# Performance work log

Measured on AMD Instinct MI355X. Metric: run time of the kernel, lower is better.

## Reference

```python
import jax, jax.numpy as jnp
import numpy as np

N_NODES = 100000
N_EDGES = 1600000
D_IN = 64
D_HID = 64


def setup_inputs() -> dict:
    key = jax.random.key(0)
    k1, k2, k3, k4, k5 = jax.random.split(key, 5)
    x = jax.random.normal(k1, (N_NODES, D_IN), dtype=jnp.float32)
    edge_index = jax.random.randint(k2, (2, N_EDGES), 0, N_NODES, dtype=jnp.int64)
    edge_weight = jax.random.uniform(k3, (N_EDGES,), dtype=jnp.float32)
    # GCNConv glorot-initialized linear weights (bias=False)
    s0 = (6.0 / (D_IN + D_HID)) ** 0.5
    W0 = jax.random.uniform(k4, (D_IN, D_HID), minval=-s0, maxval=s0, dtype=jnp.float32)
    s1 = (6.0 / (D_HID + D_HID)) ** 0.5
    W1 = jax.random.uniform(k5, (D_HID, D_HID), minval=-s1, maxval=s1, dtype=jnp.float32)
    return {"x": x, "edge_index": edge_index, "edge_weight": edge_weight, "W0": W0, "W1": W1}


def _gcn_layer(x, W, src, dst, edge_weight, deg_inv_sqrt, n_nodes):
    # h = X W  (bias=False)
    h = x @ W  # [N, D]
    # symmetric normalization including self-loops (weight 1)
    norm = deg_inv_sqrt[src] * edge_weight * deg_inv_sqrt[dst]  # [E]
    # gather src features, scale, scatter-sum at dst
    agg = jax.ops.segment_sum(norm[:, None] * h[src], dst, num_segments=n_nodes)
    # self-loop contribution: norm_ii = deg_inv_sqrt[i]^2 * 1
    agg = agg + (deg_inv_sqrt * deg_inv_sqrt)[:, None] * h
    return jax.nn.relu(agg)  # dropout is identity in eval mode


def reference(x, edge_index, edge_weight, W0, W1):
    src, dst = edge_index[0], edge_index[1]
    # degree with self-loops (self-loop weight = 1), aggregated at dst (source_to_target flow)
    deg = jax.ops.segment_sum(edge_weight, dst, num_segments=N_NODES) + 1.0
    deg_inv_sqrt = jax.lax.rsqrt(deg)
    x = _gcn_layer(x, W0, src, dst, edge_weight, deg_inv_sqrt, N_NODES)
    x = _gcn_layer(x, W1, src, dst, edge_weight, deg_inv_sqrt, N_NODES)
    return x
```

## Files before the change

kernel.cpp:

```cpp
#include <hip/hip_runtime.h>
#include <hip/hip_fp16.h>

#define D 64
#define BSH 9
#define BSZ (1 << BSH)
#define PB 4096
#define CAPR 18432
#define CAPU (2 * CAPR)
#define SCAP 9216

__global__ __launch_bounds__(256) void initcur(int* __restrict__ ccur, int nbuck) {
    int t = threadIdx.x;
    if (t < nbuck) ccur[t] = t * CAPR;
}

__global__ __launch_bounds__(512) void bucket1(const int* __restrict__ src,
                                               const int* __restrict__ dst,
                                               const float* __restrict__ ew,
                                               int* __restrict__ ccur,
                                               int2* __restrict__ pairs2,
                                               int E, int nbuck) {
    __shared__ int hist[512];
    __shared__ int lbase[512];
    __shared__ int gbase[512];
    __shared__ int w0s[PB];
    __shared__ int w1s[PB];
    __shared__ unsigned char bids[PB];
    int t = threadIdx.x;
    hist[t] = 0;
    __syncthreads();
    int e0 = blockIdx.x * PB;
    int cnt = min(PB, E - e0);
    int b[8], lr[8], w0[8], w1[8];
    int i8 = t * 8;
    bool full8 = (i8 + 8 <= cnt);
    if (full8) {
        int4   sa = *(const int4*)&src[e0 + i8];
        int4   sb = *(const int4*)&src[e0 + i8 + 4];
        int4   da = *(const int4*)&dst[e0 + i8];
        int4   db = *(const int4*)&dst[e0 + i8 + 4];
        float4 wa = *(const float4*)&ew[e0 + i8];
        float4 wb = *(const float4*)&ew[e0 + i8 + 4];
        int ss[8] = {sa.x, sa.y, sa.z, sa.w, sb.x, sb.y, sb.z, sb.w};
        int ds[8] = {da.x, da.y, da.z, da.w, db.x, db.y, db.z, db.w};
        float wv[8] = {wa.x, wa.y, wa.z, wa.w, wb.x, wb.y, wb.z, wb.w};
#pragma unroll
        for (int k = 0; k < 8; ++k) {
            b[k]  = ds[k] >> BSH;
            w0[k] = ss[k] | ((ds[k] & (BSZ - 1)) << 17);
            w1[k] = __float_as_int(wv[k]);
            lr[k] = atomicAdd(&hist[b[k]], 1);
        }
    } else {
#pragma unroll
        for (int k = 0; k < 8; ++k) {
            int idx = i8 + k;
            if (idx < cnt) {
                int d = dst[e0 + idx];
                b[k]  = d >> BSH;
                w0[k] = src[e0 + idx] | ((d & (BSZ - 1)) << 17);
                w1[k] = __float_as_int(ew[e0 + idx]);
                lr[k] = atomicAdd(&hist[b[k]], 1);
            }
        }
    }
    __syncthreads();
    int hv = hist[t];
    lbase[t] = hv;
    __syncthreads();
    for (int off = 1; off < 512; off <<= 1) {
        int u = (t >= off) ? lbase[t - off] : 0;
        __syncthreads();
        lbase[t] += u;
        __syncthreads();
    }
    int excl = lbase[t] - hv;
    __syncthreads();
    lbase[t] = excl;
    if (t < nbuck && hv > 0) gbase[t] = atomicAdd(&ccur[t], hv);
    __syncthreads();
#pragma unroll
    for (int k = 0; k < 8; ++k) {
        int idx = i8 + k;
        if (idx < cnt) {
            int slot = lbase[b[k]] + lr[k];
            w0s[slot] = w0[k];
            w1s[slot] = w1[k];
            bids[slot] = (unsigned char)b[k];
        }
    }
    __syncthreads();
    for (int i = t; i < cnt; i += 512) {
        int bb = bids[i];
        int pos = gbase[bb] + (i - lbase[bb]);
        pairs2[pos] = make_int2(w0s[i], w1s[i]);
    }
}

__global__ __launch_bounds__(512) void sort2(int2* __restrict__ pairs2,
                                             unsigned int* __restrict__ pairsU,
                                             const int* __restrict__ ccur,
                                             int2* __restrict__ rng,
                                             float* __restrict__ dis,
                                             int N, int nbuck) {
    __shared__ int2 se[SCAP];
    __shared__ int cnt[512];
    __shared__ float sdeg[512];
    __shared__ int lb[512];
    __shared__ int cur[512];
    int b = blockIdx.x;
    int t = threadIdx.x;
    int baseR = b * CAPR;
    int baseU = b * CAPU;
    int cntb = min(ccur[b] - baseR, SCAP);
    for (int i = t; i < cntb; i += 512) se[i] = pairs2[baseR + i];
    cnt[t] = 0;
    sdeg[t] = 0.0f;
    __syncthreads();
    for (int i = t; i < cntb; i += 512) {
        int2 p = se[i];
        int dl = p.x >> 17;
        atomicAdd(&cnt[dl], 1);
        atomicAdd(&sdeg[dl], __int_as_float(p.y));
    }
    __syncthreads();
    int node = (b << BSH) + t;
    int pc = (node < N) ? ((cnt[t] + 1 + 31) & ~31) : 0;
    lb[t] = pc;
    __syncthreads();
    for (int off = 1; off < 512; off <<= 1) {
        int u = (t >= off) ? lb[t - off] : 0;
        __syncthreads();
        lb[t] += u;
        __syncthreads();
    }
    int excl = lb[t] - pc;
    int totalPad = lb[511];
    float dloc = rsqrtf(sdeg[t] + 1.0f);
    __syncthreads();
    sdeg[t] = dloc;
    cur[t]  = baseU + excl;
    if (node < N) {
        rng[node] = make_int2(baseU + excl, baseU + excl + pc);
        dis[node] = dloc;
    }
    for (int i = t; i < totalPad; i += 512) pairsU[baseU + i] = 0u;
    __syncthreads();
    for (int i = t; i < cntb; i += 512) {
        int2 p = se[i];
        int dl = p.x >> 17;
        int s  = p.x & 0x1FFFF;
        int pos = atomicAdd(&cur[dl], 1);
        float w = __int_as_float(p.y) * sdeg[dl];
        unsigned int h = (unsigned int)__half_as_ushort(__float2half_rn(w));
        pairsU[pos] = ((unsigned int)s << 15) | ((h + 1u) >> 1);
    }
    __syncthreads();
    if (node < N) {
        unsigned int h = (unsigned int)__half_as_ushort(__float2half_rn(dloc));
        pairsU[cur[t]] = ((unsigned int)node << 15) | ((h + 1u) >> 1);
    }
}

__global__ __launch_bounds__(256) void gemm64h(const float* __restrict__ X,
                                               const float* __restrict__ W,
                                               const float* __restrict__ dis,
                                               __half* __restrict__ Hb, int n) {
    __shared__ float Ws[64 * 64];
    __shared__ float Xs[16 * 64];
    for (int t = threadIdx.x; t < 64 * 64; t += 256) Ws[t] = W[t];
    int row0 = blockIdx.x * 16;
    for (int t = threadIdx.x; t < 16 * 64; t += 256) {
        int r = row0 + (t >> 6);
        Xs[t] = (r < n) ? X[r * 64 + (t & 63)] : 0.0f;
    }
    __syncthreads();
    int r  = threadIdx.x >> 4;
    int jc = (threadIdx.x & 15) * 4;
    float4 acc = make_float4(0.f, 0.f, 0.f, 0.f);
#pragma unroll
    for (int k = 0; k < 64; ++k) {
        float xv = Xs[r * 64 + k];
        float4 w = *(const float4*)&Ws[k * 64 + jc];
        acc.x += xv * w.x; acc.y += xv * w.y; acc.z += xv * w.z; acc.w += xv * w.w;
    }
    int rr = row0 + r;
    if (rr < n) {
        float ds = dis[rr];
        ushort4 pk;
        pk.x = __half_as_ushort(__float2half(ds * acc.x));
        pk.y = __half_as_ushort(__float2half(ds * acc.y));
        pk.z = __half_as_ushort(__float2half(ds * acc.z));
        pk.w = __half_as_ushort(__float2half(ds * acc.w));
        *(ushort4*)&Hb[rr * 64 + jc] = pk;
    }
}

__global__ __launch_bounds__(256) void gather64(const unsigned int* __restrict__ pairs,
                                                const int2* __restrict__ rng,
                                                const __half* __restrict__ Hb,
                                                float* __restrict__ OUT, int N) {
    int node = blockIdx.x * 4 + (threadIdx.x >> 6);
    if (node >= N) return;
    int lane = threadIdx.x & 63;
    int g    = lane >> 3;
    int fl   = (lane & 7) * 8;
    int2 be = rng[node];
    __half2 z = __float2half2_rn(0.0f);
    __half2 a0[4] = {z, z, z, z};
    __half2 a1[4] = {z, z, z, z};
    __half2 a2[4] = {z, z, z, z};
    __half2 a3[4] = {z, z, z, z};
    for (int e = be.x; e < be.y; e += 32) {
        unsigned int pv = pairs[e + (lane & 31)];
        unsigned int q0 = __shfl(pv, g, 64);
        unsigned int q1 = __shfl(pv, g + 8, 64);
        unsigned int q2 = __shfl(pv, g + 16, 64);
        unsigned int q3 = __shfl(pv, g + 24, 64);
        uint4 r0 = *(const uint4*)(Hb + (size_t)(q0 >> 15) * 64 + fl);
        uint4 r1 = *(const uint4*)(Hb + (size_t)(q1 >> 15) * 64 + fl);
        uint4 r2 = *(const uint4*)(Hb + (size_t)(q2 >> 15) * 64 + fl);
        uint4 r3 = *(const uint4*)(Hb + (size_t)(q3 >> 15) * 64 + fl);
        __half2 w0 = __half2half2(__ushort_as_half((unsigned short)((q0 & 0x7FFFu) << 1)));
        __half2 w1 = __half2half2(__ushort_as_half((unsigned short)((q1 & 0x7FFFu) << 1)));
        __half2 w2 = __half2half2(__ushort_as_half((unsigned short)((q2 & 0x7FFFu) << 1)));
        __half2 w3 = __half2half2(__ushort_as_half((unsigned short)((q3 & 0x7FFFu) << 1)));
        const __half2* h0 = (const __half2*)&r0;
        const __half2* h1 = (const __half2*)&r1;
        const __half2* h2 = (const __half2*)&r2;
        const __half2* h3 = (const __half2*)&r3;
#pragma unroll
        for (int k = 0; k < 4; ++k) {
            a0[k] = __hfma2(w0, h0[k], a0[k]);
            a1[k] = __hfma2(w1, h1[k], a1[k]);
            a2[k] = __hfma2(w2, h2[k], a2[k]);
            a3[k] = __hfma2(w3, h3[k], a3[k]);
        }
    }
    __half2 a[4];
#pragma unroll
    for (int k = 0; k < 4; ++k)
        a[k] = __hadd2(__hadd2(a0[k], a1[k]), __hadd2(a2[k], a3[k]));
#pragma unroll
    for (int m = 8; m < 64; m <<= 1) {
#pragma unroll
        for (int k = 0; k < 4; ++k) {
            unsigned u = __shfl_xor(*(unsigned*)&a[k], m, 64);
            a[k] = __hadd2(a[k], *(__half2*)&u);
        }
    }
    if (g < 2) {
        int o = g * 2;
        float2 f0 = __half22float2(a[o]);
        float2 f1 = __half22float2(a[o + 1]);
        float4 vv;
        vv.x = fmaxf(f0.x, 0.0f);
        vv.y = fmaxf(f0.y, 0.0f);
        vv.z = fmaxf(f1.x, 0.0f);
        vv.w = fmaxf(f1.y, 0.0f);
        *(float4*)&OUT[node * 64 + fl + g * 4] = vv;
    }
}

extern "C" void kernel_launch(void* const* d_in, const int* in_sizes, int n_in,
                              void* d_out, int out_size, void* d_ws, size_t ws_size,
                              hipStream_t stream) {
    const float* x  = (const float*)d_in[0];
    const int*   ei = (const int*)d_in[1];
    const float* ew = (const float*)d_in[2];
    const float* W0 = (const float*)d_in[3];
    const float* W1 = (const float*)d_in[4];
    float* out = (float*)d_out;

    const int N = in_sizes[0] / D;
    const int E = in_sizes[2];
    const int* src = ei;
    const int* dst = ei + E;

    const int nbuck = (N + BSZ - 1) >> BSH;
    const int Na = (N + 1 + 255) & ~255;

    float* dis     = (float*)d_ws;
    int2*  rng     = (int2*)((int*)d_ws + Na);
    int*   ccur    = (int*)d_ws + 3 * Na;
    int2*  pairs2  = (int2*)((int*)d_ws + 3 * Na + 1024);
    unsigned int* pairsU = (unsigned int*)pairs2;
    __half* Hb     = (__half*)((int*)d_ws + 3 * Na + 1024 + (size_t)nbuck * CAPU);

    const int nb1 = (E + PB - 1) / PB;

    initcur<<<1, 256, 0, stream>>>(ccur, nbuck);
    bucket1<<<nb1, 512, 0, stream>>>(src, dst, ew, ccur, pairs2, E, nbuck);
    sort2<<<nbuck, 512, 0, stream>>>(pairs2, pairsU, ccur, rng, dis, N, nbuck);

    const int gemm_grid   = (N + 15) / 16;
    const int gather_grid = (N + 3) / 4;

    gemm64h<<<gemm_grid, 256, 0, stream>>>(x, W0, dis, Hb, N);
    gather64<<<gather_grid, 256, 0, stream>>>(pairsU, rng, Hb, out, N);

    gemm64h<<<gemm_grid, 256, 0, stream>>>(out, W1, dis, Hb, N);
    gather64<<<gather_grid, 256, 0, stream>>>(pairsU, rng, Hb, out, N);
}
```

Measured before the change: 195.7 us.

## Make gather persistent and process two nodes per wave for overlapped loads

The gather kernel now launches a fixed grid of 8192 waves that loop over nodes with a grid-stride. Each iteration handles two nodes and issues the first edge chunk of both before finishing either, aiming to overlap the latency of the irregular gathers. The four separate per-slot accumulators become one chained accumulator per node, which serialises the FMA dependencies. The first chunk is read unconditionally, which relies on padded pair storage or on nodes always having edges.

```diff
diff --git a/kernel.cpp b/kernel.cpp
--- a/kernel.cpp
+++ b/kernel.cpp
@@ -8,6 +8,7 @@
 #define CAPR 18432
 #define CAPU (2 * CAPR)
 #define SCAP 9216
+#define GWAVES 8192
 
 __global__ __launch_bounds__(256) void initcur(int* __restrict__ ccur, int nbuck) {
     int t = threadIdx.x;
@@ -196,51 +197,36 @@
     }
 }
 
-__global__ __launch_bounds__(256) void gather64(const unsigned int* __restrict__ pairs,
-                                                const int2* __restrict__ rng,
-                                                const __half* __restrict__ Hb,
-                                                float* __restrict__ OUT, int N) {
-    int node = blockIdx.x * 4 + (threadIdx.x >> 6);
-    if (node >= N) return;
-    int lane = threadIdx.x & 63;
-    int g    = lane >> 3;
-    int fl   = (lane & 7) * 8;
-    int2 be = rng[node];
-    __half2 z = __float2half2_rn(0.0f);
-    __half2 a0[4] = {z, z, z, z};
-    __half2 a1[4] = {z, z, z, z};
-    __half2 a2[4] = {z, z, z, z};
-    __half2 a3[4] = {z, z, z, z};
-    for (int e = be.x; e < be.y; e += 32) {
-        unsigned int pv = pairs[e + (lane & 31)];
-        unsigned int q0 = __shfl(pv, g, 64);
-        unsigned int q1 = __shfl(pv, g + 8, 64);
-        unsigned int q2 = __shfl(pv, g + 16, 64);
-        unsigned int q3 = __shfl(pv, g + 24, 64);
-        uint4 r0 = *(const uint4*)(Hb + (size_t)(q0 >> 15) * 64 + fl);
-        uint4 r1 = *(const uint4*)(Hb + (size_t)(q1 >> 15) * 64 + fl);
-        uint4 r2 = *(const uint4*)(Hb + (size_t)(q2 >> 15) * 64 + fl);
-        uint4 r3 = *(const uint4*)(Hb + (size_t)(q3 >> 15) * 64 + fl);
-        __half2 w0 = __half2half2(__ushort_as_half((unsigned short)((q0 & 0x7FFFu) << 1)));
-        __half2 w1 = __half2half2(__ushort_as_half((unsigned short)((q1 & 0x7FFFu) << 1)));
-        __half2 w2 = __half2half2(__ushort_as_half((unsigned short)((q2 & 0x7FFFu) << 1)));
-        __half2 w3 = __half2half2(__ushort_as_half((unsigned short)((q3 & 0x7FFFu) << 1)));
-        const __half2* h0 = (const __half2*)&r0;
-        const __half2* h1 = (const __half2*)&r1;
-        const __half2* h2 = (const __half2*)&r2;
-        const __half2* h3 = (const __half2*)&r3;
-#pragma unroll
-        for (int k = 0; k < 4; ++k) {
-            a0[k] = __hfma2(w0, h0[k], a0[k]);
-            a1[k] = __hfma2(w1, h1[k], a1[k]);
-            a2[k] = __hfma2(w2, h2[k], a2[k]);
-            a3[k] = __hfma2(w3, h3[k], a3[k]);
-        }
-    }
-    __half2 a[4];
-#pragma unroll
-    for (int k = 0; k < 4; ++k)
-        a[k] = __hadd2(__hadd2(a0[k], a1[k]), __hadd2(a2[k], a3[k]));
+__device__ __forceinline__ void acc_group(unsigned int pv, int g, int fl,
+                                          const __half* __restrict__ Hb,
+                                          __half2 a[4]) {
+    unsigned int q0 = __shfl(pv, g, 64);
+    unsigned int q1 = __shfl(pv, g + 8, 64);
+    unsigned int q2 = __shfl(pv, g + 16, 64);
+    unsigned int q3 = __shfl(pv, g + 24, 64);
+    uint4 r0 = *(const uint4*)(Hb + (size_t)(q0 >> 15) * 64 + fl);
+    uint4 r1 = *(const uint4*)(Hb + (size_t)(q1 >> 15) * 64 + fl);
+    uint4 r2 = *(const uint4*)(Hb + (size_t)(q2 >> 15) * 64 + fl);
+    uint4 r3 = *(const uint4*)(Hb + (size_t)(q3 >> 15) * 64 + fl);
+    __half2 w0 = __half2half2(__ushort_as_half((unsigned short)((q0 & 0x7FFFu) << 1)));
+    __half2 w1 = __half2half2(__ushort_as_half((unsigned short)((q1 & 0x7FFFu) << 1)));
+    __half2 w2 = __half2half2(__ushort_as_half((unsigned short)((q2 & 0x7FFFu) << 1)));
+    __half2 w3 = __half2half2(__ushort_as_half((unsigned short)((q3 & 0x7FFFu) << 1)));
+    const __half2* h0 = (const __half2*)&r0;
+    const __half2* h1 = (const __half2*)&r1;
+    const __half2* h2 = (const __half2*)&r2;
+    const __half2* h3 = (const __half2*)&r3;
+#pragma unroll
+    for (int k = 0; k < 4; ++k) {
+        a[k] = __hfma2(w0, h0[k], a[k]);
+        a[k] = __hfma2(w1, h1[k], a[k]);
+        a[k] = __hfma2(w2, h2[k], a[k]);
+        a[k] = __hfma2(w3, h3[k], a[k]);
+    }
+}
+
+__device__ __forceinline__ void finish_node(__half2 a[4], int g, int fl,
+                                            float* __restrict__ OUT, int node) {
 #pragma unroll
     for (int m = 8; m < 64; m <<= 1) {
 #pragma unroll
@@ -262,6 +248,36 @@
     }
 }
 
+__global__ __launch_bounds__(256) void gather64(const unsigned int* __restrict__ pairs,
+                                                const int2* __restrict__ rng,
+                                                const __half* __restrict__ Hb,
+                                                float* __restrict__ OUT, int N) {
+    int wid  = blockIdx.x * 4 + (threadIdx.x >> 6);
+    int lane = threadIdx.x & 63;
+    int g    = lane >> 3;
+    int fl   = (lane & 7) * 8;
+    int l31  = lane & 31;
+    __half2 z = __float2half2_rn(0.0f);
+    for (int n0 = wid; n0 < N; n0 += 2 * GWAVES) {
+        int n1 = n0 + GWAVES;
+        bool h1 = (n1 < N);
+        int2 be0 = rng[n0];
+        int2 be1 = h1 ? rng[n1] : be0;
+        unsigned int pv0 = pairs[be0.x + l31];
+        unsigned int pv1 = pairs[be1.x + l31];
+        __half2 a0[4] = {z, z, z, z};
+        __half2 a1[4] = {z, z, z, z};
+        acc_group(pv0, g, fl, Hb, a0);
+        acc_group(pv1, g, fl, Hb, a1);
+        for (int e = be0.x + 32; e < be0.y; e += 32)
+            acc_group(pairs[e + l31], g, fl, Hb, a0);
+        for (int e = be1.x + 32; e < be1.y; e += 32)
+            acc_group(pairs[e + l31], g, fl, Hb, a1);
+        finish_node(a0, g, fl, OUT, n0);
+        if (h1) finish_node(a1, g, fl, OUT, n1);
+    }
+}
+
 extern "C" void kernel_launch(void* const* d_in, const int* in_sizes, int n_in,
                               void* d_out, int out_size, void* d_ws, size_t ws_size,
                               hipStream_t stream) {
@@ -294,7 +310,7 @@
     sort2<<<nbuck, 512, 0, stream>>>(pairs2, pairsU, ccur, rng, dis, N, nbuck);
 
     const int gemm_grid   = (N + 15) / 16;
-    const int gather_grid = (N + 3) / 4;
+    const int gather_grid = GWAVES / 4;
 
     gemm64h<<<gemm_grid, 256, 0, stream>>>(x, W0, dis, Hb, N);
     gather64<<<gather_grid, 256, 0, stream>>>(pairsU, rng, Hb, out, N);
```

Result: slower. 203.6 us (+4.0%).
